# Kernel optimization log

Measured on AMD Instinct MI355X. Metric: run time of the kernel, lower is better.

Reference implementation:

```python
import jax, jax.numpy as jnp
import numpy as np

N_NODES = 50000
N_FEAT = 128
DIM = 10
N_EDGES = 1600000
N_GRAPHS = 1000


def setup_inputs() -> dict:
    key = jax.random.key(0)
    ks = jax.random.split(key, 8)
    x = jax.random.normal(ks[0], (N_NODES, N_FEAT), dtype=jnp.float32)
    W1_l = jax.random.normal(ks[1], (DIM, N_FEAT), dtype=jnp.float32) * 0.1
    W1_r = jax.random.normal(ks[2], (DIM, N_FEAT), dtype=jnp.float32) * 0.1
    W2_l = jax.random.normal(ks[3], (DIM, DIM), dtype=jnp.float32) * 0.3
    W2_r = jax.random.normal(ks[4], (DIM, DIM), dtype=jnp.float32) * 0.3
    Wfc = jax.random.normal(ks[5], (1, DIM), dtype=jnp.float32) * 0.3
    edge_index = jax.random.randint(ks[6], (2, N_EDGES), 0, N_NODES, dtype=jnp.int64)
    batch = jnp.sort(jax.random.randint(ks[7], (N_NODES,), 0, N_GRAPHS, dtype=jnp.int64))
    return {"x": x, "W1_l": W1_l, "W1_r": W1_r, "W2_l": W2_l, "W2_r": W2_r,
            "Wfc": Wfc, "edge_index": edge_index, "batch": batch}


def _sage_conv(h, src, dst, deg_inv, Wl, Wr):
    # mean aggregation over incoming neighbors, then two bias-free linears
    agg = jax.ops.segment_sum(h[src], dst, num_segments=N_NODES)  # [N, F]
    agg = agg * deg_inv[:, None]
    return agg @ Wl.T + h @ Wr.T


def reference(x, W1_l, W1_r, W2_l, W2_r, Wfc, edge_index, batch):
    src, dst = edge_index[0], edge_index[1]
    # in-degree per destination node (mean denominator, clamped at 1 like PyG)
    deg = jax.ops.segment_sum(jnp.ones((src.shape[0],), x.dtype), dst, num_segments=N_NODES)
    deg_inv = 1.0 / jnp.maximum(deg, 1.0)

    h = jax.nn.relu(_sage_conv(x, src, dst, deg_inv, W1_l, W1_r))
    h = _sage_conv(h, src, dst, deg_inv, W2_l, W2_r)

    # global mean pool over graphs
    counts = jax.ops.segment_sum(jnp.ones((N_NODES,), x.dtype), batch, num_segments=N_GRAPHS)
    pooled = jax.ops.segment_sum(h, batch, num_segments=N_GRAPHS)
    pooled = pooled / jnp.maximum(counts, 1.0)[:, None]

    return jax.nn.sigmoid(pooled @ Wfc.T)  # [N_GRAPHS, 1]
```

## Files before the change

### kernel.cpp

```cpp
#include <hip/hip_runtime.h>
#include <hip/hip_bf16.h>
#include <math.h>

#define N_NODES  50000
#define N_FEAT   128
#define DIM      10
#define N_EDGES  1600000
#define N_GRAPHS 1000
#define PSTRIDE  16
#define CAP      80
#define BSH      8
#define NBUCK    196
#define BCAP     9216
#define ACHUNK   8192
#define ABLOCKS  ((N_EDGES + ACHUNK - 1) / ACHUNK)
#define PBLOCKS  ((N_NODES + 255) / 256)
#define SPLIT    8
#define GSLOTS   128
#define SENT     50000

__device__ __forceinline__ float bf2f(unsigned short u) {
    union { unsigned int i; float f; } v;
    v.i = ((unsigned int)u) << 16;
    return v.f;
}

__device__ __forceinline__ float wload(const void* w, int fm, int i) {
    return fm ? ((const float*)w)[i] : bf2f(((const unsigned short*)w)[i]);
}

__device__ __forceinline__ int iload(const void* p, int im, long long pos) {
    return im ? (int)((const long long*)p)[pos] : ((const int*)p)[pos];
}

__global__ void detect_setup_kernel(
    const unsigned short* __restrict__ w1l, const unsigned int* __restrict__ ei32,
    const void* __restrict__ W2l, const void* __restrict__ W2r,
    const void* __restrict__ Wfc,
    int* __restrict__ fmode, int* __restrict__ imode,
    float* __restrict__ vl, float* __restrict__ vr,
    int* __restrict__ bcur, float* __restrict__ gsum, float* __restrict__ gcnt,
    float* __restrict__ p) {
    __shared__ int bigcnt, oddnz;
    if (threadIdx.x == 0) { bigcnt = 0; oddnz = 0; }
    __syncthreads();
    for (int i = threadIdx.x; i < DIM * N_FEAT; i += 256) {
        int expo = (w1l[i] >> 7) & 0xFF;
        if (expo >= 0x90) atomicAdd(&bigcnt, 1);
    }
    for (int i = threadIdx.x; i < 2048; i += 256) {
        if (ei32[2 * i + 1] != 0) atomicAdd(&oddnz, 1);
    }
    for (int i = threadIdx.x; i < NBUCK; i += 256) bcur[i] = 0;
    for (int i = threadIdx.x; i < N_GRAPHS; i += 256) { gsum[i] = 0.f; gcnt[i] = 0.f; }
    if (threadIdx.x < PSTRIDE) p[(size_t)SENT * PSTRIDE + threadIdx.x] = 0.f;
    __syncthreads();
    int fm = (bigcnt >= 4) ? 1 : 0;
    if (threadIdx.x == 0) { *fmode = fm; *imode = (oddnz == 0) ? 1 : 0; }
    int j = threadIdx.x;
    if (j < DIM) {
        float al = 0.f, ar = 0.f;
        for (int i = 0; i < DIM; i++) {
            float w = wload(Wfc, fm, i);
            al += w * wload(W2l, fm, i * DIM + j);
            ar += w * wload(W2r, fm, i * DIM + j);
        }
        vl[j] = al;
        vr[j] = ar;
    } else if (j < 16) {
        vl[j] = 0.f;
        vr[j] = 0.f;
    }
}

#define ACCUM8(f0)                                                  \
    _Pragma("unroll")                                               \
    for (int d = 0; d < DIM; d++) {                                 \
        _Pragma("unroll")                                           \
        for (int k = 0; k < 8; k++) {                               \
            accl[d] += xf[k] * wl[d * N_FEAT + (f0) + k];           \
            accr[d] += xf[k] * wr[d * N_FEAT + (f0) + k];           \
        }                                                           \
    }

__global__ __launch_bounds__(256) void fusedA_kernel(
    const void* __restrict__ ei, const void* __restrict__ x,
    const void* __restrict__ W1l, const void* __restrict__ W1r,
    const int* __restrict__ fmode, const int* __restrict__ imode,
    int* __restrict__ bcur, unsigned int* __restrict__ bedges,
    float* __restrict__ p, float* __restrict__ q) {
    __shared__ union U {
        struct { unsigned int stage[ACHUNK]; int hcnt[NBUCK]; int hbase[NBUCK]; } a;
        struct { float wl[DIM * N_FEAT]; float wr[DIM * N_FEAT]; } b;
    } sh;

    if (blockIdx.x < ABLOCKS) {
        int im = *imode;
        for (int b = threadIdx.x; b < NBUCK; b += 256) sh.a.hcnt[b] = 0;
        __syncthreads();
        long long e0 = (long long)blockIdx.x * ACHUNK;
        int nE = (int)min((long long)ACHUNK, (long long)N_EDGES - e0);
        for (int i = threadIdx.x; i < nE; i += 256) {
            int s = iload(ei, im, e0 + i);
            int d = iload(ei, im, (long long)N_EDGES + e0 + i);
            sh.a.stage[i] = (unsigned)s | ((unsigned)(d & 255) << 16) | ((unsigned)(d >> BSH) << 24);
            atomicAdd(&sh.a.hcnt[d >> BSH], 1);
        }
        __syncthreads();
        for (int b = threadIdx.x; b < NBUCK; b += 256) {
            int c = sh.a.hcnt[b];
            sh.a.hbase[b] = c ? atomicAdd(&bcur[b], c) : 0;
            sh.a.hcnt[b] = 0;
        }
        __syncthreads();
        for (int i = threadIdx.x; i < nE; i += 256) {
            unsigned rec = sh.a.stage[i];
            int b = rec >> 24;
            int pos = sh.a.hbase[b] + atomicAdd(&sh.a.hcnt[b], 1);
            if (pos < BCAP) bedges[(size_t)b * BCAP + pos] = rec;
        }
    } else {
        int fm = *fmode;
        float* wl = sh.b.wl;
        float* wr = sh.b.wr;
        for (int i = threadIdx.x; i < DIM * N_FEAT; i += 256) {
            wl[i] = wload(W1l, fm, i);
            wr[i] = wload(W1r, fm, i);
        }
        __syncthreads();
        int n = (blockIdx.x - ABLOCKS) * 256 + threadIdx.x;
        if (n >= N_NODES) return;

        float accl[DIM], accr[DIM];
#pragma unroll
        for (int d = 0; d < DIM; d++) { accl[d] = 0.f; accr[d] = 0.f; }

        if (fm) {
            const float4* xr = reinterpret_cast<const float4*>((const float*)x + (size_t)n * N_FEAT);
            for (int fb = 0; fb < N_FEAT / 8; fb++) {
                float4 v0 = xr[2 * fb];
                float4 v1 = xr[2 * fb + 1];
                float xf[8] = {v0.x, v0.y, v0.z, v0.w, v1.x, v1.y, v1.z, v1.w};
                ACCUM8(fb * 8)
            }
        } else {
            const uint4* xr = reinterpret_cast<const uint4*>((const unsigned short*)x + (size_t)n * N_FEAT);
            for (int fb = 0; fb < N_FEAT / 8; fb++) {
                uint4 v = xr[fb];
                float xf[8];
                xf[0] = bf2f((unsigned short)(v.x & 0xffff)); xf[1] = bf2f((unsigned short)(v.x >> 16));
                xf[2] = bf2f((unsigned short)(v.y & 0xffff)); xf[3] = bf2f((unsigned short)(v.y >> 16));
                xf[4] = bf2f((unsigned short)(v.z & 0xffff)); xf[5] = bf2f((unsigned short)(v.z >> 16));
                xf[6] = bf2f((unsigned short)(v.w & 0xffff)); xf[7] = bf2f((unsigned short)(v.w >> 16));
                ACCUM8(fb * 8)
            }
        }
        float* pr = p + (size_t)n * PSTRIDE;
        float* qr = q + (size_t)n * PSTRIDE;
#pragma unroll
        for (int d = 0; d < DIM; d++) { pr[d] = accl[d]; qr[d] = accr[d]; }
#pragma unroll
        for (int d = DIM; d < PSTRIDE; d++) { pr[d] = 0.f; qr[d] = 0.f; }
    }
}

__global__ __launch_bounds__(1024) void binB_kernel(
    const int* __restrict__ bcur, const unsigned int* __restrict__ bedges,
    int* __restrict__ cnt, unsigned short* __restrict__ col) {
    __shared__ unsigned short lcol[256 * CAP];
    __shared__ int lcnt[256];
    const unsigned int s2 = (unsigned)SENT | ((unsigned)SENT << 16);
    uint4 sv = make_uint4(s2, s2, s2, s2);
    uint4* l4 = reinterpret_cast<uint4*>(lcol);
    for (int i = threadIdx.x; i < 256 * CAP * 2 / 16; i += 1024) l4[i] = sv;
    if (threadIdx.x < 256) lcnt[threadIdx.x] = 0;
    __syncthreads();
    int b = blockIdx.x;
    int m = min(bcur[b], BCAP);
    const unsigned int* seg = bedges + (size_t)b * BCAP;
    for (int i = threadIdx.x; i < m; i += 1024) {
        unsigned rec = seg[i];
        int nidx = (rec >> 16) & 255;
        int pos = atomicAdd(&lcnt[nidx], 1);
        if (pos < CAP) lcol[nidx * CAP + pos] = (unsigned short)(rec & 0xffffu);
    }
    __syncthreads();
    int node0 = b << BSH;
    int nvalid = min(256, N_NODES - node0);
    if ((int)threadIdx.x < nvalid) cnt[node0 + threadIdx.x] = lcnt[threadIdx.x];
    int total = nvalid * CAP / 8;
    uint4* dst4 = (uint4*)(col + (size_t)node0 * CAP);
    const uint4* src4 = (const uint4*)lcol;
    for (int i = threadIdx.x; i < total; i += 1024) dst4[i] = src4[i];
}

__global__ __launch_bounds__(256) void pull1_kernel(
    const int* __restrict__ cnt, const unsigned short* __restrict__ col,
    const float* __restrict__ p, const float* __restrict__ q,
    const float* __restrict__ vl, const float* __restrict__ vr,
    float* __restrict__ t, float* __restrict__ u, float* __restrict__ dinv) {
    int g = blockIdx.x * 64 + (threadIdx.x >> 2);
    int sub4 = (threadIdx.x & 3) * 4;
    if (g >= N_NODES) return;
    int deg = cnt[g];
    int dcl = min(deg, CAP);
    const unsigned short* cl = col + (size_t)g * CAP;
    float ax = 0.f, ay = 0.f, az = 0.f, aw = 0.f;
    for (int k0 = 0; k0 < dcl; k0 += 8) {
        uint4 cv = *reinterpret_cast<const uint4*>(cl + k0);
        unsigned c[8];
        c[0] = cv.x & 0xffff; c[1] = cv.x >> 16;
        c[2] = cv.y & 0xffff; c[3] = cv.y >> 16;
        c[4] = cv.z & 0xffff; c[5] = cv.z >> 16;
        c[6] = cv.w & 0xffff; c[7] = cv.w >> 16;
#pragma unroll
        for (int j = 0; j < 8; j++) {
            const float4 v = *reinterpret_cast<const float4*>(p + (size_t)c[j] * PSTRIDE + sub4);
            ax += v.x; ay += v.y; az += v.z; aw += v.w;
        }
    }
    float di = 1.0f / fmaxf((float)deg, 1.0f);
    float4 qv  = *reinterpret_cast<const float4*>(q + (size_t)g * PSTRIDE + sub4);
    float4 vlv = *reinterpret_cast<const float4*>(vl + sub4);
    float4 vrv = *reinterpret_cast<const float4*>(vr + sub4);
    float hx = fmaxf(ax * di + qv.x, 0.f);
    float hy = fmaxf(ay * di + qv.y, 0.f);
    float hz = fmaxf(az * di + qv.z, 0.f);
    float hw = fmaxf(aw * di + qv.w, 0.f);
    float tv = hx * vlv.x + hy * vlv.y + hz * vlv.z + hw * vlv.w;
    float uv = hx * vrv.x + hy * vrv.y + hz * vrv.z + hw * vrv.w;
    tv += __shfl_xor(tv, 1, 4); tv += __shfl_xor(tv, 2, 4);
    uv += __shfl_xor(uv, 1, 4); uv += __shfl_xor(uv, 2, 4);
    if (sub4 == 0) {
        t[g] = tv;
        u[g] = uv;
        dinv[g] = di;
    }
}

__global__ __launch_bounds__(256) void pull2B_kernel(
    const int* __restrict__ bcur, const unsigned int* __restrict__ bedges,
    const float* __restrict__ t, const float* __restrict__ u,
    const float* __restrict__ dinv, const void* __restrict__ batch,
    const int* __restrict__ imode,
    float* __restrict__ gsum, float* __restrict__ gcnt) {
    __shared__ float ldinv[256];
    __shared__ int   lb[256];
    __shared__ float lgs[GSLOTS];
    __shared__ float lgc[GSLOTS];
    int b = blockIdx.x / SPLIT;
    int s = blockIdx.x % SPLIT;
    int tid = threadIdx.x;
    int node0 = b << BSH;
    int nvalid = min(256, N_NODES - node0);
    int im = *imode;
    if (tid < nvalid) {
        ldinv[tid] = dinv[node0 + tid];
        lb[tid] = iload(batch, im, node0 + tid);
    }
    if (tid < GSLOTS) { lgs[tid] = 0.f; lgc[tid] = 0.f; }
    __syncthreads();
    int g0 = lb[0];
    int rng = lb[nvalid - 1] - g0 + 1;
    bool useLDS = (rng <= GSLOTS);
    int m = min(bcur[b], BCAP);
    int c0 = (m * s) / SPLIT, c1 = (m * (s + 1)) / SPLIT;
    const unsigned int* seg = bedges + (size_t)b * BCAP;
    for (int i = c0 + tid; i < c1; i += 256) {
        unsigned rec = seg[i];
        int src  = rec & 0xffffu;
        int nidx = (rec >> 16) & 255;
        float val = t[src] * ldinv[nidx];
        int gg = lb[nidx];
        if (useLDS) atomicAdd(&lgs[gg - g0], val);
        else        atomicAdd(gsum + gg, val);
    }
    if (s == 0 && tid < nvalid) {
        int gg = lb[tid];
        float uval = u[node0 + tid];
        if (useLDS) {
            atomicAdd(&lgs[gg - g0], uval);
            atomicAdd(&lgc[gg - g0], 1.0f);
        } else {
            atomicAdd(gsum + gg, uval);
            atomicAdd(gcnt + gg, 1.0f);
        }
    }
    __syncthreads();
    if (useLDS) {
        for (int i = tid; i < rng; i += 256) {
            float v = lgs[i];
            if (v != 0.f) atomicAdd(gsum + g0 + i, v);
            if (s == 0) {
                float c = lgc[i];
                if (c != 0.f) atomicAdd(gcnt + g0 + i, c);
            }
        }
    }
}

__global__ __launch_bounds__(256) void final_kernel(
    const float* __restrict__ gsum, const float* __restrict__ gcnt,
    const int* __restrict__ fmode, void* __restrict__ out) {
    int g = blockIdx.x * 256 + threadIdx.x;
    if (g >= N_GRAPHS) return;
    float pooled = gsum[g] / fmaxf(gcnt[g], 1.0f);
    float sg = 1.0f / (1.0f + expf(-pooled));
    if (*fmode) {
        ((float*)out)[g] = sg;
    } else {
        ((__hip_bfloat16*)out)[g] = __float2bfloat16(sg);
    }
}

extern "C" void kernel_launch(void* const* d_in, const int* in_sizes, int n_in,
                              void* d_out, int out_size, void* d_ws, size_t ws_size,
                              hipStream_t stream) {
    const void* x    = d_in[0];
    const void* W1l  = d_in[1];
    const void* W1r  = d_in[2];
    const void* W2l  = d_in[3];
    const void* W2r  = d_in[4];
    const void* Wfc  = d_in[5];
    const void* ei   = d_in[6];
    const void* batc = d_in[7];

    char* ws = (char*)d_ws;
    int*   fmode = (int*)ws;
    int*   imode = fmode + 1;
    float* vl   = (float*)(ws + 64);
    float* vr   = vl + 16;
    int*   bcur = (int*)(vr + 16);
    float* gsum = (float*)(bcur + NBUCK);
    float* gcnt = gsum + N_GRAPHS;
    unsigned int* bedges = (unsigned int*)(ws + ((((size_t)(gcnt + N_GRAPHS) - (size_t)ws) + 255) & ~(size_t)255));
    int*   cnt  = (int*)(bedges + (size_t)NBUCK * BCAP);
    unsigned short* col = (unsigned short*)(cnt + N_NODES);
    float* p    = (float*)(col + (size_t)N_NODES * CAP);
    float* q    = p + (size_t)(N_NODES + 1) * PSTRIDE;
    float* t    = q + (size_t)N_NODES * PSTRIDE;
    float* u    = t + N_NODES;
    float* dinv = u + N_NODES;

    detect_setup_kernel<<<1, 256, 0, stream>>>(
        (const unsigned short*)W1l, (const unsigned int*)ei, W2l, W2r, Wfc,
        fmode, imode, vl, vr, bcur, gsum, gcnt, p);
    fusedA_kernel<<<ABLOCKS + PBLOCKS, 256, 0, stream>>>(
        ei, x, W1l, W1r, fmode, imode, bcur, bedges, p, q);
    binB_kernel<<<NBUCK, 1024, 0, stream>>>(bcur, bedges, cnt, col);
    pull1_kernel<<<(N_NODES * 4 + 255) / 256, 256, 0, stream>>>(cnt, col, p, q, vl, vr, t, u, dinv);
    pull2B_kernel<<<NBUCK * SPLIT, 256, 0, stream>>>(bcur, bedges, t, u, dinv, batc, imode, gsum, gcnt);
    final_kernel<<<(N_GRAPHS + 255) / 256, 256, 0, stream>>>(gsum, gcnt, fmode, d_out);
}
```

Before: 164.7 us.

## Split node projection across four lanes per node and halve edge binning chunk

The node-projection part of the fused kernel now gives each node to four lanes. Each lane handles an interleaved quarter of the 128 features, and the partial sums are combined with xor shuffles. Lane 0 writes the padded p/q rows as float4 stores. Separately, the edge-binning chunk size is halved, which doubles the number of edge blocks. Together these raise parallelism and memory-level concurrency in the first phase, at the cost of more shuffles, more LDS weight loads per block and more atomics on the bucket counters.

Measured after the change: 161.8 us. No clear change (-1.8%).

```diff
diff --git a/kernel.cpp b/kernel.cpp
--- a/kernel.cpp
+++ b/kernel.cpp
@@ -12,9 +12,9 @@
 #define BSH      8
 #define NBUCK    196
 #define BCAP     9216
-#define ACHUNK   8192
+#define ACHUNK   4096
 #define ABLOCKS  ((N_EDGES + ACHUNK - 1) / ACHUNK)
-#define PBLOCKS  ((N_NODES + 255) / 256)
+#define PBLOCKS4 ((N_NODES * 4 + 255) / 256)
 #define SPLIT    8
 #define GSLOTS   128
 #define SENT     50000
@@ -128,7 +128,9 @@
             wr[i] = wload(W1r, fm, i);
         }
         __syncthreads();
-        int n = (blockIdx.x - ABLOCKS) * 256 + threadIdx.x;
+        int tid4 = (blockIdx.x - ABLOCKS) * 256 + threadIdx.x;
+        int n = tid4 >> 2;
+        int sub = tid4 & 3;
         if (n >= N_NODES) return;
 
         float accl[DIM], accr[DIM];
@@ -137,7 +139,9 @@
 
         if (fm) {
             const float4* xr = reinterpret_cast<const float4*>((const float*)x + (size_t)n * N_FEAT);
-            for (int fb = 0; fb < N_FEAT / 8; fb++) {
+#pragma unroll
+            for (int j = 0; j < 4; j++) {
+                int fb = j * 4 + sub;
                 float4 v0 = xr[2 * fb];
                 float4 v1 = xr[2 * fb + 1];
                 float xf[8] = {v0.x, v0.y, v0.z, v0.w, v1.x, v1.y, v1.z, v1.w};
@@ -145,7 +149,9 @@
             }
         } else {
             const uint4* xr = reinterpret_cast<const uint4*>((const unsigned short*)x + (size_t)n * N_FEAT);
-            for (int fb = 0; fb < N_FEAT / 8; fb++) {
+#pragma unroll
+            for (int j = 0; j < 4; j++) {
+                int fb = j * 4 + sub;
                 uint4 v = xr[fb];
                 float xf[8];
                 xf[0] = bf2f((unsigned short)(v.x & 0xffff)); xf[1] = bf2f((unsigned short)(v.x >> 16));
@@ -155,12 +161,25 @@
                 ACCUM8(fb * 8)
             }
         }
-        float* pr = p + (size_t)n * PSTRIDE;
-        float* qr = q + (size_t)n * PSTRIDE;
-#pragma unroll
-        for (int d = 0; d < DIM; d++) { pr[d] = accl[d]; qr[d] = accr[d]; }
-#pragma unroll
-        for (int d = DIM; d < PSTRIDE; d++) { pr[d] = 0.f; qr[d] = 0.f; }
+#pragma unroll
+        for (int d = 0; d < DIM; d++) {
+            accl[d] += __shfl_xor(accl[d], 1, 4);
+            accl[d] += __shfl_xor(accl[d], 2, 4);
+            accr[d] += __shfl_xor(accr[d], 1, 4);
+            accr[d] += __shfl_xor(accr[d], 2, 4);
+        }
+        if (sub == 0) {
+            float4* pr = reinterpret_cast<float4*>(p + (size_t)n * PSTRIDE);
+            float4* qr = reinterpret_cast<float4*>(q + (size_t)n * PSTRIDE);
+            pr[0] = make_float4(accl[0], accl[1], accl[2], accl[3]);
+            pr[1] = make_float4(accl[4], accl[5], accl[6], accl[7]);
+            pr[2] = make_float4(accl[8], accl[9], 0.f, 0.f);
+            pr[3] = make_float4(0.f, 0.f, 0.f, 0.f);
+            qr[0] = make_float4(accr[0], accr[1], accr[2], accr[3]);
+            qr[1] = make_float4(accr[4], accr[5], accr[6], accr[7]);
+            qr[2] = make_float4(accr[8], accr[9], 0.f, 0.f);
+            qr[3] = make_float4(0.f, 0.f, 0.f, 0.f);
+        }
     }
 }
 
@@ -345,7 +364,7 @@
     detect_setup_kernel<<<1, 256, 0, stream>>>(
         (const unsigned short*)W1l, (const unsigned int*)ei, W2l, W2r, Wfc,
         fmode, imode, vl, vr, bcur, gsum, gcnt, p);
-    fusedA_kernel<<<ABLOCKS + PBLOCKS, 256, 0, stream>>>(
+    fusedA_kernel<<<ABLOCKS + PBLOCKS4, 256, 0, stream>>>(
         ei, x, W1l, W1r, fmode, imode, bcur, bedges, p, q);
     binB_kernel<<<NBUCK, 1024, 0, stream>>>(bcur, bedges, cnt, col);
     pull1_kernel<<<(N_NODES * 4 + 255) / 256, 256, 0, stream>>>(cnt, col, p, q, vl, vr, t, u, dinv);
```
